# Kernel optimization log

Measured on AMD Instinct MI355X. Metric: run time of the kernel, lower is better.

The kernel has to match this reference:

```python
import jax, jax.numpy as jnp
import numpy as np

V = 50000
E = 500000
D = 128


def setup_inputs() -> dict:
    key = jax.random.key(0)
    k1, k2, k3, k4, k5, k6 = jax.random.split(key, 6)
    edge_feats = jax.random.normal(k1, (E, D), dtype=jnp.float32)
    node_feats = jax.random.normal(k2, (V, 1), dtype=jnp.float32)
    edge_index = jax.random.randint(k3, (2, E), 0, V, dtype=jnp.int64)
    rev_index = jax.random.randint(k4, (E,), 0, E, dtype=jnp.int64)
    # Linear(hidden_dim, hidden_dim, bias=True) params, Kaiming-uniform-ish init
    lim = 1.0 / np.sqrt(D)
    W = jax.random.uniform(k5, (D, D), dtype=jnp.float32, minval=-lim, maxval=lim)
    b = jax.random.uniform(k6, (D,), dtype=jnp.float32, minval=-lim, maxval=lim)
    return {"edge_feats": edge_feats, "node_feats": node_feats, "W": W, "b": b,
            "edge_index": edge_index, "rev_index": rev_index}


def reference(edge_feats, node_feats, W, b, edge_index, rev_index):
    src, dest = edge_index[0], edge_index[1]
    messages = jax.nn.relu(edge_feats)                      # [E, d]
    # scatter-sum messages onto destination nodes
    node_messages = jax.ops.segment_sum(messages, dest, num_segments=node_feats.shape[0])  # [V, d]
    # gather back to edges, subtract reverse-edge message (D-MPNN)
    edge_messages = node_messages[src] - messages[rev_index]  # [E, d]
    # update: Linear (dropout p=0.0 is identity)
    return edge_messages @ W.T + b
```

## Files before the change

kernel.cpp:

```cpp
#include <hip/hip_runtime.h>

#define DD 128
#define TILE_E 64
#define LDW 136

typedef __attribute__((ext_vector_type(8))) short short8;
typedef __attribute__((ext_vector_type(4))) float f32x4;

__device__ __forceinline__ unsigned short f2bf(float f) {
  unsigned int u = __float_as_uint(f);
  u += 0x7FFF + ((u >> 16) & 1);
  return (unsigned short)(u >> 16);
}


__global__ __launch_bounds__(256) void hist_kernel(
    const int* __restrict__ eidx, int* __restrict__ cnt, int E) {
  int e = blockIdx.x * 256 + threadIdx.x;
  if (e < E) atomicAdd(&cnt[eidx[E + e]], 1);
}

__global__ __launch_bounds__(1024) void scan_kernel(
    const int* __restrict__ cnt, int* __restrict__ off, int* __restrict__ cur, int V) {
  __shared__ int s[1024];
  const int t = threadIdx.x;
  const int chunk = (V + 1023) / 1024;
  const int lo = t * chunk, hi = min(lo + chunk, V);
  int tot = 0;
  for (int v = lo; v < hi; ++v) tot += cnt[v];
  s[t] = tot;
  __syncthreads();
  for (int d = 1; d < 1024; d <<= 1) {
    int x = (t >= d) ? s[t - d] : 0;
    __syncthreads();
    s[t] += x;
    __syncthreads();
  }
  int run = (t > 0) ? s[t - 1] : 0;
  for (int v = lo; v < hi; ++v) {
    off[v] = run; cur[v] = run;
    run += cnt[v];
  }
}

__global__ __launch_bounds__(256) void fill_kernel(
    const int* __restrict__ eidx, int* __restrict__ cur,
    int* __restrict__ elist, int E) {
  int e = blockIdx.x * 256 + threadIdx.x;
  if (e < E) {
    int p = atomicAdd(&cur[eidx[E + e]], 1);
    elist[p] = e;
  }
}

__global__ __launch_bounds__(256) void gather_sum_kernel(
    const float* __restrict__ ef, const int* __restrict__ off,
    const int* __restrict__ cnt, const int* __restrict__ elist,
    float* __restrict__ nm, int V) {
  const int lane = threadIdx.x & 63;
  const int v = blockIdx.x * 4 + (threadIdx.x >> 6);
  if (v >= V) return;
  const int base = off[v];
  const int deg  = cnt[v];
  float2 acc = make_float2(0.f, 0.f);
  for (int j = 0; j < deg; ++j) {
    int e = elist[base + j];
    float2 m = ((const float2*)(ef + (size_t)e * DD))[lane];
    acc.x += fmaxf(m.x, 0.f);
    acc.y += fmaxf(m.y, 0.f);
  }
  ((float2*)(nm + (size_t)v * DD))[lane] = acc;
}

__global__ __launch_bounds__(256) void wconv_kernel(
    const float* __restrict__ W, unsigned short* __restrict__ Wbf) {
  int idx = blockIdx.x * 256 + threadIdx.x;
  if (idx >= DD * DD / 4) return;
  float4 w = ((const float4*)W)[idx];
  unsigned int lo = f2bf(w.x) | ((unsigned int)f2bf(w.y) << 16);
  unsigned int hi = f2bf(w.z) | ((unsigned int)f2bf(w.w) << 16);
  *(uint2*)&Wbf[idx * 4] = make_uint2(lo, hi);
}

__global__ __launch_bounds__(256) void fused_gather_gemm_kernel(
    const float* __restrict__ ef, const float* __restrict__ nm,
    const unsigned short* __restrict__ Wbf, const float* __restrict__ bias,
    const int* __restrict__ eidx, const int* __restrict__ rev,
    float* __restrict__ out, int E) {
  __shared__ __align__(16) unsigned short Wl[DD * LDW];
  __shared__ __align__(16) unsigned short Al[TILE_E * LDW];
  const int tid = threadIdx.x;

  #pragma unroll
  for (int i = 0; i < 8; ++i) {
    int idx = tid + i * 256;
    int n   = idx >> 4;
    int k8  = idx & 15;
    uint4 w = ((const uint4*)Wbf)[idx];
    *(uint4*)&Wl[n * LDW + (k8 << 3)] = w;
  }

  const int e0 = blockIdx.x * TILE_E;
  {
    int el = tid >> 2;
    int kb = (tid & 3) << 3;
    int e  = e0 + el;
    int s = 0, rv = 0;
    if (e < E) { s = eidx[e]; rv = rev[e]; }
    const float4* nmp = (const float4*)(nm + (size_t)s  * DD);
    const float4* efp = (const float4*)(ef + (size_t)rv * DD);
    #pragma unroll
    for (int i = 0; i < 8; ++i) {
      int k4 = kb + i;
      float4 a = nmp[k4];
      float4 m = efp[k4];
      float x0 = a.x - fmaxf(m.x, 0.f);
      float x1 = a.y - fmaxf(m.y, 0.f);
      float x2 = a.z - fmaxf(m.z, 0.f);
      float x3 = a.w - fmaxf(m.w, 0.f);
      unsigned int lo = f2bf(x0) | ((unsigned int)f2bf(x1) << 16);
      unsigned int hi = f2bf(x2) | ((unsigned int)f2bf(x3) << 16);
      *(uint2*)&Al[el * LDW + (k4 << 2)] = make_uint2(lo, hi);
    }
  }
  __syncthreads();

  const int lane = tid & 63;
  const int wave = tid >> 6;
  const int col  = lane & 15;
  const int quad = lane >> 4;
  const int erow = wave * 16;

  f32x4 acc[8];
  #pragma unroll
  for (int i = 0; i < 8; ++i) acc[i] = (f32x4){0.f, 0.f, 0.f, 0.f};

  #pragma unroll
  for (int kt = 0; kt < 4; ++kt) {
    const int k0 = kt * 32 + quad * 8;
    short8 a = *(const short8*)&Al[(erow + col) * LDW + k0];
    #pragma unroll
    for (int nt = 0; nt < 8; ++nt) {
      short8 b = *(const short8*)&Wl[(nt * 16 + col) * LDW + k0];
      acc[nt] = __builtin_amdgcn_mfma_f32_16x16x32_bf16(a, b, acc[nt], 0, 0, 0);
    }
  }

  #pragma unroll
  for (int nt = 0; nt < 8; ++nt) {
    float bj = bias[nt * 16 + col];
    #pragma unroll
    for (int r = 0; r < 4; ++r) {
      int e = e0 + erow + quad * 4 + r;
      if (e < E) out[(size_t)e * DD + nt * 16 + col] = acc[nt][r] + bj;
    }
  }
}

extern "C" void kernel_launch(void* const* d_in, const int* in_sizes, int n_in,
                              void* d_out, int out_size, void* d_ws, size_t ws_size,
                              hipStream_t stream) {
  const float* ef   = (const float*)d_in[0];
  const float* W    = (const float*)d_in[2];
  const float* bias = (const float*)d_in[3];
  const int*   eidx = (const int*)d_in[4];
  const int*   rev  = (const int*)d_in[5];
  float*       out  = (float*)d_out;

  const int V = in_sizes[1];
  const int E = in_sizes[5];

  char* ws = (char*)d_ws;
  size_t o = 0;
  float* nm = (float*)(ws + o);            o += (size_t)V * DD * sizeof(float);
  o = (o + 255) & ~(size_t)255;
  int* cnt  = (int*)(ws + o);              o += (size_t)V * sizeof(int);
  o = (o + 255) & ~(size_t)255;
  int* off  = (int*)(ws + o);              o += (size_t)V * sizeof(int);
  o = (o + 255) & ~(size_t)255;
  int* cur  = (int*)(ws + o);              o += (size_t)V * sizeof(int);
  o = (o + 255) & ~(size_t)255;
  int* elist = (int*)(ws + o);             o += (size_t)E * sizeof(int);
  o = (o + 255) & ~(size_t)255;
  unsigned short* Wbf = (unsigned short*)(ws + o);

  hipMemsetAsync(cnt, 0, (size_t)V * sizeof(int), stream);

  int eb = (E + 255) / 256;
  hist_kernel<<<eb, 256, 0, stream>>>(eidx, cnt, E);
  scan_kernel<<<1, 1024, 0, stream>>>(cnt, off, cur, V);
  fill_kernel<<<eb, 256, 0, stream>>>(eidx, cur, elist, E);
  gather_sum_kernel<<<(V + 3) / 4, 256, 0, stream>>>(ef, off, cnt, elist, nm, V);
  wconv_kernel<<<(DD * DD / 4 + 255) / 256, 256, 0, stream>>>(W, Wbf);

  int nblocks = (E + TILE_E - 1) / TILE_E;
  fused_gather_gemm_kernel<<<nblocks, 256, 0, stream>>>(ef, nm, Wbf, bias, eidx, rev, out, E);
}
```

Measured before the change: 778.3 us.

## Drop LDS staging in fused GEMM, pre-swizzle W into MFMA fragment order

The weight conversion kernel now writes W in bf16, already laid out in the per-lane MFMA B-fragment order. The fused kernel then loads A and B operands straight from global memory into registers, with no shared-memory staging and no __syncthreads. This removes the per-block 34KB+ LDS writes of W and A and the barrier, which also raises occupancy (launch bounds set to 4). The gather-sum loop is unrolled by 4 with two accumulators to put more loads in flight. The trade-off is that W is now re-read from L2 by every wave instead of being shared through LDS.

```diff
diff --git a/kernel.cpp b/kernel.cpp
--- a/kernel.cpp
+++ b/kernel.cpp
@@ -2,7 +2,6 @@
 
 #define DD 128
 #define TILE_E 64
-#define LDW 136
 
 typedef __attribute__((ext_vector_type(8))) short short8;
 typedef __attribute__((ext_vector_type(4))) float f32x4;
@@ -62,74 +61,70 @@
   if (v >= V) return;
   const int base = off[v];
   const int deg  = cnt[v];
-  float2 acc = make_float2(0.f, 0.f);
-  for (int j = 0; j < deg; ++j) {
+  float2 acc0 = make_float2(0.f, 0.f);
+  float2 acc1 = make_float2(0.f, 0.f);
+  int j = 0;
+  for (; j + 4 <= deg; j += 4) {
+    int ea = elist[base + j + 0];
+    int eb = elist[base + j + 1];
+    int ec = elist[base + j + 2];
+    int ed = elist[base + j + 3];
+    float2 ma = ((const float2*)(ef + (size_t)ea * DD))[lane];
+    float2 mb = ((const float2*)(ef + (size_t)eb * DD))[lane];
+    float2 mc = ((const float2*)(ef + (size_t)ec * DD))[lane];
+    float2 md = ((const float2*)(ef + (size_t)ed * DD))[lane];
+    acc0.x += fmaxf(ma.x, 0.f) + fmaxf(mb.x, 0.f);
+    acc0.y += fmaxf(ma.y, 0.f) + fmaxf(mb.y, 0.f);
+    acc1.x += fmaxf(mc.x, 0.f) + fmaxf(md.x, 0.f);
+    acc1.y += fmaxf(mc.y, 0.f) + fmaxf(md.y, 0.f);
+  }
+  for (; j < deg; ++j) {
     int e = elist[base + j];
     float2 m = ((const float2*)(ef + (size_t)e * DD))[lane];
-    acc.x += fmaxf(m.x, 0.f);
-    acc.y += fmaxf(m.y, 0.f);
-  }
-  ((float2*)(nm + (size_t)v * DD))[lane] = acc;
+    acc0.x += fmaxf(m.x, 0.f);
+    acc0.y += fmaxf(m.y, 0.f);
+  }
+  ((float2*)(nm + (size_t)v * DD))[lane] =
+      make_float2(acc0.x + acc1.x, acc0.y + acc1.y);
 }
 
 __global__ __launch_bounds__(256) void wconv_kernel(
-    const float* __restrict__ W, unsigned short* __restrict__ Wbf) {
+    const float* __restrict__ W, unsigned short* __restrict__ Wswz) {
   int idx = blockIdx.x * 256 + threadIdx.x;
-  if (idx >= DD * DD / 4) return;
-  float4 w = ((const float4*)W)[idx];
-  unsigned int lo = f2bf(w.x) | ((unsigned int)f2bf(w.y) << 16);
-  unsigned int hi = f2bf(w.z) | ((unsigned int)f2bf(w.w) << 16);
-  *(uint2*)&Wbf[idx * 4] = make_uint2(lo, hi);
-}
-
-__global__ __launch_bounds__(256) void fused_gather_gemm_kernel(
+  if (idx >= DD * DD / 8) return;
+  int lane = idx & 63;
+  int nt   = (idx >> 6) & 7;
+  int kt   = idx >> 9;
+  int n = nt * 16 + (lane & 15);
+  int k = kt * 32 + (lane >> 4) * 8;
+  const float4* wrow = (const float4*)(W + (size_t)n * DD + k);
+  float4 w0 = wrow[0];
+  float4 w1 = wrow[1];
+  unsigned int p0 = f2bf(w0.x) | ((unsigned int)f2bf(w0.y) << 16);
+  unsigned int p1 = f2bf(w0.z) | ((unsigned int)f2bf(w0.w) << 16);
+  unsigned int p2 = f2bf(w1.x) | ((unsigned int)f2bf(w1.y) << 16);
+  unsigned int p3 = f2bf(w1.z) | ((unsigned int)f2bf(w1.w) << 16);
+  ((uint4*)Wswz)[idx] = make_uint4(p0, p1, p2, p3);
+}
+
+__global__ __launch_bounds__(256, 4) void fused_gather_gemm_kernel(
     const float* __restrict__ ef, const float* __restrict__ nm,
-    const unsigned short* __restrict__ Wbf, const float* __restrict__ bias,
+    const unsigned short* __restrict__ Wswz, const float* __restrict__ bias,
     const int* __restrict__ eidx, const int* __restrict__ rev,
     float* __restrict__ out, int E) {
-  __shared__ __align__(16) unsigned short Wl[DD * LDW];
-  __shared__ __align__(16) unsigned short Al[TILE_E * LDW];
-  const int tid = threadIdx.x;
-
-  #pragma unroll
-  for (int i = 0; i < 8; ++i) {
-    int idx = tid + i * 256;
-    int n   = idx >> 4;
-    int k8  = idx & 15;
-    uint4 w = ((const uint4*)Wbf)[idx];
-    *(uint4*)&Wl[n * LDW + (k8 << 3)] = w;
-  }
-
-  const int e0 = blockIdx.x * TILE_E;
-  {
-    int el = tid >> 2;
-    int kb = (tid & 3) << 3;
-    int e  = e0 + el;
-    int s = 0, rv = 0;
-    if (e < E) { s = eidx[e]; rv = rev[e]; }
-    const float4* nmp = (const float4*)(nm + (size_t)s  * DD);
-    const float4* efp = (const float4*)(ef + (size_t)rv * DD);
-    #pragma unroll
-    for (int i = 0; i < 8; ++i) {
-      int k4 = kb + i;
-      float4 a = nmp[k4];
-      float4 m = efp[k4];
-      float x0 = a.x - fmaxf(m.x, 0.f);
-      float x1 = a.y - fmaxf(m.y, 0.f);
-      float x2 = a.z - fmaxf(m.z, 0.f);
-      float x3 = a.w - fmaxf(m.w, 0.f);
-      unsigned int lo = f2bf(x0) | ((unsigned int)f2bf(x1) << 16);
-      unsigned int hi = f2bf(x2) | ((unsigned int)f2bf(x3) << 16);
-      *(uint2*)&Al[el * LDW + (k4 << 2)] = make_uint2(lo, hi);
-    }
-  }
-  __syncthreads();
-
+  const int tid  = threadIdx.x;
   const int lane = tid & 63;
   const int wave = tid >> 6;
   const int col  = lane & 15;
   const int quad = lane >> 4;
-  const int erow = wave * 16;
+  const int e0   = blockIdx.x * TILE_E + wave * 16;
+
+  const int ea = e0 + col;
+  int s = 0, rv = 0;
+  if (ea < E) { s = eidx[ea]; rv = rev[ea]; }
+  const float4* __restrict__ nmp = (const float4*)(nm + (size_t)s  * DD);
+  const float4* __restrict__ efp = (const float4*)(ef + (size_t)rv * DD);
+  const short8* __restrict__ wp  = (const short8*)Wswz + lane;
 
   f32x4 acc[8];
   #pragma unroll
@@ -137,11 +132,28 @@
 
   #pragma unroll
   for (int kt = 0; kt < 4; ++kt) {
-    const int k0 = kt * 32 + quad * 8;
-    short8 a = *(const short8*)&Al[(erow + col) * LDW + k0];
+    const int k4 = kt * 8 + quad * 2;
+    float4 a0 = nmp[k4];
+    float4 a1 = nmp[k4 + 1];
+    float4 m0 = efp[k4];
+    float4 m1 = efp[k4 + 1];
+    float x0 = a0.x - fmaxf(m0.x, 0.f);
+    float x1 = a0.y - fmaxf(m0.y, 0.f);
+    float x2 = a0.z - fmaxf(m0.z, 0.f);
+    float x3 = a0.w - fmaxf(m0.w, 0.f);
+    float x4 = a1.x - fmaxf(m1.x, 0.f);
+    float x5 = a1.y - fmaxf(m1.y, 0.f);
+    float x6 = a1.z - fmaxf(m1.z, 0.f);
+    float x7 = a1.w - fmaxf(m1.w, 0.f);
+    union { unsigned int u[4]; short8 s8; } cvt;
+    cvt.u[0] = f2bf(x0) | ((unsigned int)f2bf(x1) << 16);
+    cvt.u[1] = f2bf(x2) | ((unsigned int)f2bf(x3) << 16);
+    cvt.u[2] = f2bf(x4) | ((unsigned int)f2bf(x5) << 16);
+    cvt.u[3] = f2bf(x6) | ((unsigned int)f2bf(x7) << 16);
+    short8 a = cvt.s8;
     #pragma unroll
     for (int nt = 0; nt < 8; ++nt) {
-      short8 b = *(const short8*)&Wl[(nt * 16 + col) * LDW + k0];
+      short8 b = wp[(kt * 8 + nt) * 64];
       acc[nt] = __builtin_amdgcn_mfma_f32_16x16x32_bf16(a, b, acc[nt], 0, 0, 0);
     }
   }
@@ -151,7 +163,7 @@
     float bj = bias[nt * 16 + col];
     #pragma unroll
     for (int r = 0; r < 4; ++r) {
-      int e = e0 + erow + quad * 4 + r;
+      int e = e0 + quad * 4 + r;
       if (e < E) out[(size_t)e * DD + nt * 16 + col] = acc[nt][r] + bj;
     }
   }
@@ -182,7 +194,7 @@
   o = (o + 255) & ~(size_t)255;
   int* elist = (int*)(ws + o);             o += (size_t)E * sizeof(int);
   o = (o + 255) & ~(size_t)255;
-  unsigned short* Wbf = (unsigned short*)(ws + o);
+  unsigned short* Wswz = (unsigned short*)(ws + o);
 
   hipMemsetAsync(cnt, 0, (size_t)V * sizeof(int), stream);
 
@@ -191,8 +203,8 @@
   scan_kernel<<<1, 1024, 0, stream>>>(cnt, off, cur, V);
   fill_kernel<<<eb, 256, 0, stream>>>(eidx, cur, elist, E);
   gather_sum_kernel<<<(V + 3) / 4, 256, 0, stream>>>(ef, off, cnt, elist, nm, V);
-  wconv_kernel<<<(DD * DD / 4 + 255) / 256, 256, 0, stream>>>(W, Wbf);
+  wconv_kernel<<<(DD * DD / 8 + 255) / 256, 256, 0, stream>>>(W, Wswz);
 
   int nblocks = (E + TILE_E - 1) / TILE_E;
-  fused_gather_gemm_kernel<<<nblocks, 256, 0, stream>>>(ef, nm, Wbf, bias, eidx, rev, out, E);
-}
+  fused_gather_gemm_kernel<<<nblocks, 256, 0, stream>>>(ef, nm, Wswz, bias, eidx, rev, out, E);
+}
```

Measured after the change: 740.2 us. -4.9%, faster.
